# Optimization experiments

Measured on AMD Instinct MI355X. Metric: run time of the kernel, lower is better.

The kernel has to match this reference:

```python
import jax, jax.numpy as jnp
import numpy as np

COS_EPS = 1e-8    # torch.nn.CosineSimilarity default eps
NORM_EPS = 1e-12  # torch F.normalize default eps


def _cosine_gram(x, y):
    # Pairwise cosine similarity as a GEMM over row-normalized vectors,
    # matching torch: dot / max(|x|*|y|, eps). Avoids O(b^2*d) broadcast.
    dots = x @ y.T                               # [b, b]
    nx = jnp.linalg.norm(x, axis=1)              # [b]
    ny = jnp.linalg.norm(y, axis=1)              # [b]
    return dots / jnp.maximum(nx[:, None] * ny[None, :], COS_EPS)


def _row_normalize(g):
    # torch F.normalize(p=2, dim=1): x / max(||x||, eps)
    n = jnp.linalg.norm(g, axis=1, keepdims=True)
    return g / jnp.maximum(n, NORM_EPS)


def setup_inputs() -> dict:
    key = jax.random.key(0)
    k1, k2, k3, k4 = jax.random.split(key, 4)
    bsz, dim = 8192, 128
    return {
        "zxs": jax.random.normal(k1, (bsz, dim), dtype=jnp.float32),
        "zys": jax.random.normal(k2, (bsz, dim), dtype=jnp.float32),
        "zxt": jax.random.normal(k3, (bsz, dim), dtype=jnp.float32),
        "zyt": jax.random.normal(k4, (bsz, dim), dtype=jnp.float32),
        "temperature": jnp.asarray(0.5, dtype=jnp.float32),
    }


def reference(zxs, zys, zxt, zyt, temperature):
    bsz = zxs.shape[0]
    sim_s = _row_normalize(_cosine_gram(zxs, zys) / temperature)  # [b, b]
    sim_t = _row_normalize(_cosine_gram(zxt, zyt) / temperature)  # [b, b]
    g_diff = sim_t - sim_s
    loss = jnp.sum(g_diff * g_diff) / (bsz * bsz)
    return loss
```

## Files before the change

kernel.cpp:

```cpp
#include <hip/hip_runtime.h>
#include <hip/hip_bf16.h>


typedef __attribute__((ext_vector_type(8))) short short8;
typedef __attribute__((ext_vector_type(4))) float float4v;

#define BSZ 8192
#define DIM 128
#define NP  128
#define KROWS 64
#define PITCH 72
#define INV_B2 1.4901161193847656e-08f

__device__ __forceinline__ short f2bf(float x) {
    union { __hip_bfloat16 b; short s; } u;
    u.b = __float2bfloat16(x);
    return u.s;
}

__global__ __launch_bounds__(256, 3) void gram_g(
    const float* __restrict__ Yt, const float* __restrict__ Ys,
    float* __restrict__ partial)
{
    __shared__ short T[2][128 * PITCH];
    __shared__ float rsum[2][KROWS];
    __shared__ float invn[KROWS];

    const int tid   = threadIdx.x;
    const int lane  = tid & 63;
    const int wave  = tid >> 6;
    const int d     = tid & 127;
    const int khalf = tid >> 7;
    const int q     = lane >> 4;
    const int l15   = lane & 15;
    const int split = blockIdx.x;
    const int gram  = blockIdx.y;

    auto stage_mat = [&](int m, const float* __restrict__ Y) {
        float v[32];
        const float* base = Y + ((size_t)(split * KROWS + khalf * 32)) * DIM + d;
        #pragma unroll
        for (int i = 0; i < 32; ++i) v[i] = base[(size_t)i * DIM];

        #pragma unroll
        for (int i = 0; i < 32; ++i) {
            float ss = v[i] * v[i];
            #pragma unroll
            for (int off = 1; off < 64; off <<= 1) ss += __shfl_xor(ss, off);
            if (lane == 0) rsum[wave & 1][khalf * 32 + i] = ss;
        }
        __syncthreads();
        if (tid < KROWS) {
            float s = rsum[0][tid] + rsum[1][tid];
            invn[tid] = (s > 0.f) ? rsqrtf(s) : 0.f;
        }
        __syncthreads();

        #pragma unroll
        for (int g = 0; g < 4; ++g) {
            short8 pk;
            #pragma unroll
            for (int j = 0; j < 8; ++j) {
                int i = g * 8 + j;
                pk[j] = f2bf(v[i] * invn[khalf * 32 + i]);
            }
            *(short8*)&T[m][d * PITCH + khalf * 32 + g * 8] = pk;
        }
    };

    if (gram == 0) {
        stage_mat(0, Yt);
    } else if (gram == 1) {
        stage_mat(0, Ys);
    } else {
        stage_mat(0, Yt);
        __syncthreads();
        stage_mat(1, Ys);
    }
    __syncthreads();

    const short* TA = T[0];
    const short* TB = (gram == 2) ? T[1] : T[0];

    float4v acc[2][8];
    #pragma unroll
    for (int a = 0; a < 2; ++a)
        #pragma unroll
        for (int b = 0; b < 8; ++b) acc[a][b] = (float4v){0.f, 0.f, 0.f, 0.f};

    #pragma unroll
    for (int kk = 0; kk < 2; ++kk) {
        short8 fb[8], fa[2];
        #pragma unroll
        for (int s = 0; s < 8; ++s)
            fb[s] = *(const short8*)&TB[(s * 16 + l15) * PITCH + kk * 32 + q * 8];
        #pragma unroll
        for (int a = 0; a < 2; ++a)
            fa[a] = *(const short8*)&TA[((wave * 2 + a) * 16 + l15) * PITCH + kk * 32 + q * 8];
        #pragma unroll
        for (int a = 0; a < 2; ++a)
            #pragma unroll
            for (int b = 0; b < 8; ++b)
                acc[a][b] = __builtin_amdgcn_mfma_f32_16x16x32_bf16(
                    fa[a], fb[b], acc[a][b], 0, 0, 0);
    }

    float* P = partial + ((size_t)(gram * NP + split) << 14);
    #pragma unroll
    for (int a = 0; a < 2; ++a) {
        int strip = wave * 2 + a;
        #pragma unroll
        for (int b = 0; b < 8; ++b)
            #pragma unroll
            for (int r = 0; r < 4; ++r)
                P[((strip * 16 + q * 4 + r) << 7) + b * 16 + l15] = acc[a][b][r];
    }
}

__global__ __launch_bounds__(256) void reduce_g(
    const float* __restrict__ partial, __hip_bfloat16* __restrict__ Gb)
{
    int o = blockIdx.x * 256 + threadIdx.x;
    int g = o >> 14, rem = o & 16383;
    float s = 0.f;
    for (int b = 0; b < NP; ++b)
        s += partial[((size_t)(g * NP + b) << 14) + rem];
    int d1 = rem >> 7, d2 = rem & 127;
    Gb[(g << 14) + (d2 << 7) + d1] = __float2bfloat16(s);
}

__global__ __launch_bounds__(256) void quad_k(
    const float* __restrict__ Xt, const float* __restrict__ Xs,
    const __hip_bfloat16* __restrict__ Gb, float* __restrict__ out)
{
    const int tid  = threadIdx.x;
    const int lane = tid & 63;
    const int wave = tid >> 6;
    const int q    = lane >> 4;
    const int l15  = lane & 15;
    const int rbase = blockIdx.x * 64 + wave * 16;

    short8 At[4], As[4];
    #pragma unroll
    for (int kk = 0; kk < 4; ++kk) {
        const float* pt = Xt + (size_t)(rbase + l15) * DIM + kk * 32 + q * 8;
        const float* ps = Xs + (size_t)(rbase + l15) * DIM + kk * 32 + q * 8;
        float4 t0 = *(const float4*)pt, t1 = *(const float4*)(pt + 4);
        float4 s0 = *(const float4*)ps, s1 = *(const float4*)(ps + 4);
        short8 a, b;
        a[0]=f2bf(t0.x); a[1]=f2bf(t0.y); a[2]=f2bf(t0.z); a[3]=f2bf(t0.w);
        a[4]=f2bf(t1.x); a[5]=f2bf(t1.y); a[6]=f2bf(t1.z); a[7]=f2bf(t1.w);
        b[0]=f2bf(s0.x); b[1]=f2bf(s0.y); b[2]=f2bf(s0.z); b[3]=f2bf(s0.w);
        b[4]=f2bf(s1.x); b[5]=f2bf(s1.y); b[6]=f2bf(s1.z); b[7]=f2bf(s1.w);
        At[kk] = a; As[kk] = b;
    }

    float fA[4] = {0,0,0,0}, fB[4] = {0,0,0,0}, fC[4] = {0,0,0,0};
    const short* G = (const short*)Gb;

    #pragma unroll
    for (int nt = 0; nt < 8; ++nt) {
        int d2 = nt * 16 + l15;
        float4v qt = {0.f,0.f,0.f,0.f}, qs = qt, qc = qt;
        #pragma unroll
        for (int kk = 0; kk < 4; ++kk) {
            int off = (d2 << 7) + kk * 32 + q * 8;
            short8 Bt = *(const short8*)&G[off];
            short8 Bs = *(const short8*)&G[16384 + off];
            short8 Bm = *(const short8*)&G[32768 + off];
            qt = __builtin_amdgcn_mfma_f32_16x16x32_bf16(At[kk], Bt, qt, 0, 0, 0);
            qs = __builtin_amdgcn_mfma_f32_16x16x32_bf16(As[kk], Bs, qs, 0, 0, 0);
            qc = __builtin_amdgcn_mfma_f32_16x16x32_bf16(At[kk], Bm, qc, 0, 0, 0);
        }
        #pragma unroll
        for (int r = 0; r < 4; ++r) {
            int row = rbase + q * 4 + r;
            float xtv = Xt[(size_t)row * DIM + d2];
            float xsv = Xs[(size_t)row * DIM + d2];
            fA[r] += qt[r] * xtv;
            fB[r] += qs[r] * xsv;
            fC[r] += qc[r] * xsv;
        }
    }

    float wl = 0.f;
    #pragma unroll
    for (int r = 0; r < 4; ++r) {
        float A = fA[r], B = fB[r], C = fC[r];
        #pragma unroll
        for (int off = 1; off < 16; off <<= 1) {
            A += __shfl_xor(A, off);
            B += __shfl_xor(B, off);
            C += __shfl_xor(C, off);
        }
        float contrib = 2.f - 2.f * C * rsqrtf(A * B);
        wl += (l15 == 0) ? contrib : 0.f;
    }
    wl += __shfl_xor(wl, 16);
    wl += __shfl_xor(wl, 32);

    __shared__ float wred[4];
    if (lane == 0) wred[wave] = wl;
    __syncthreads();
    if (tid == 0)
        atomicAdd(out, (wred[0] + wred[1] + wred[2] + wred[3]) * INV_B2);
}

extern "C" void kernel_launch(void* const* d_in, const int* in_sizes, int n_in,
                              void* d_out, int out_size, void* d_ws, size_t ws_size,
                              hipStream_t stream) {
    const float* zxs = (const float*)d_in[0];
    const float* zys = (const float*)d_in[1];
    const float* zxt = (const float*)d_in[2];
    const float* zyt = (const float*)d_in[3];
    float* out = (float*)d_out;

    char* ws = (char*)d_ws;
    float* partial = (float*)ws;
    __hip_bfloat16* Gb = (__hip_bfloat16*)(ws + (size_t)3 * NP * 16384 * sizeof(float));

    hipMemsetAsync(out, 0, sizeof(float), stream);
    dim3 ggrid(NP, 3);
    gram_g  <<<ggrid, 256, 0, stream>>>(zyt, zys, partial);
    reduce_g<<<192,   256, 0, stream>>>(partial, Gb);
    quad_k  <<<128,   256, 0, stream>>>(zxt, zxs, Gb, out);
}
```

Before: 112.7 us.

## Split normalization into prep kernel, halve gram partials, drop memset

Adds a prep kernel that normalizes the Y rows once, converts them to bf16 and writes them transposed to workspace. The gram kernel then loads these fragments directly from global memory, using 512 threads and 128 K-rows per block. This removes the Yt/Ys normalization that the cross-gram blocks repeated and halves the partial buffer that reduce_g must sum. The output is now zeroed inside prep, replacing the memset. The cost is an extra launch plus a global round trip for the transposed data, and strided, uncached-looking global fragment loads in gram_g.

```diff
diff --git a/kernel.cpp b/kernel.cpp
--- a/kernel.cpp
+++ b/kernel.cpp
@@ -7,9 +7,7 @@
 
 #define BSZ 8192
 #define DIM 128
-#define NP  128
-#define KROWS 64
-#define PITCH 72
+#define NP  64
 #define INV_B2 1.4901161193847656e-08f
 
 __device__ __forceinline__ short f2bf(float x) {
@@ -18,103 +16,94 @@
     return u.s;
 }
 
-__global__ __launch_bounds__(256, 3) void gram_g(
+__global__ __launch_bounds__(256) void prep(
     const float* __restrict__ Yt, const float* __restrict__ Ys,
-    float* __restrict__ partial)
-{
-    __shared__ short T[2][128 * PITCH];
-    __shared__ float rsum[2][KROWS];
-    __shared__ float invn[KROWS];
+    short* __restrict__ YT, float* __restrict__ out)
+{
+    __shared__ float rsum[2][64];
+    __shared__ float invn[64];
 
     const int tid   = threadIdx.x;
     const int lane  = tid & 63;
     const int wave  = tid >> 6;
     const int d     = tid & 127;
     const int khalf = tid >> 7;
-    const int q     = lane >> 4;
-    const int l15   = lane & 15;
+    const int chunk = blockIdx.x;
+    const int mat   = blockIdx.y;
+    const float* Y  = mat ? Ys : Yt;
+
+    if (chunk == 0 && mat == 0 && tid == 0) out[0] = 0.f;
+
+    float v[32];
+    const float* base = Y + (size_t)(chunk * 64 + khalf * 32) * DIM + d;
+    #pragma unroll
+    for (int i = 0; i < 32; ++i) v[i] = base[(size_t)i * DIM];
+
+    #pragma unroll
+    for (int i = 0; i < 32; ++i) {
+        float ss = v[i] * v[i];
+        #pragma unroll
+        for (int off = 1; off < 64; off <<= 1) ss += __shfl_xor(ss, off);
+        if (lane == 0) rsum[wave & 1][khalf * 32 + i] = ss;
+    }
+    __syncthreads();
+    if (tid < 64) {
+        float s = rsum[0][tid] + rsum[1][tid];
+        invn[tid] = (s > 0.f) ? rsqrtf(s) : 0.f;
+    }
+    __syncthreads();
+
+    short* yt = YT + ((size_t)mat * 128 + d) * BSZ + chunk * 64 + khalf * 32;
+    #pragma unroll
+    for (int g = 0; g < 4; ++g) {
+        short8 pk;
+        #pragma unroll
+        for (int j = 0; j < 8; ++j) {
+            int i = g * 8 + j;
+            pk[j] = f2bf(v[i] * invn[khalf * 32 + i]);
+        }
+        *(short8*)&yt[g * 8] = pk;
+    }
+}
+
+__global__ __launch_bounds__(512) void gram_g(
+    const short* __restrict__ YT, float* __restrict__ partial)
+{
+    const int tid  = threadIdx.x;
+    const int lane = tid & 63;
+    const int s1   = tid >> 6;
+    const int q    = lane >> 4;
+    const int l15  = lane & 15;
     const int split = blockIdx.x;
     const int gram  = blockIdx.y;
 
-    auto stage_mat = [&](int m, const float* __restrict__ Y) {
-        float v[32];
-        const float* base = Y + ((size_t)(split * KROWS + khalf * 32)) * DIM + d;
-        #pragma unroll
-        for (int i = 0; i < 32; ++i) v[i] = base[(size_t)i * DIM];
-
-        #pragma unroll
-        for (int i = 0; i < 32; ++i) {
-            float ss = v[i] * v[i];
-            #pragma unroll
-            for (int off = 1; off < 64; off <<= 1) ss += __shfl_xor(ss, off);
-            if (lane == 0) rsum[wave & 1][khalf * 32 + i] = ss;
-        }
-        __syncthreads();
-        if (tid < KROWS) {
-            float s = rsum[0][tid] + rsum[1][tid];
-            invn[tid] = (s > 0.f) ? rsqrtf(s) : 0.f;
-        }
-        __syncthreads();
-
-        #pragma unroll
-        for (int g = 0; g < 4; ++g) {
-            short8 pk;
-            #pragma unroll
-            for (int j = 0; j < 8; ++j) {
-                int i = g * 8 + j;
-                pk[j] = f2bf(v[i] * invn[khalf * 32 + i]);
-            }
-            *(short8*)&T[m][d * PITCH + khalf * 32 + g * 8] = pk;
-        }
-    };
-
-    if (gram == 0) {
-        stage_mat(0, Yt);
-    } else if (gram == 1) {
-        stage_mat(0, Ys);
-    } else {
-        stage_mat(0, Yt);
-        __syncthreads();
-        stage_mat(1, Ys);
-    }
-    __syncthreads();
-
-    const short* TA = T[0];
-    const short* TB = (gram == 2) ? T[1] : T[0];
-
-    float4v acc[2][8];
-    #pragma unroll
-    for (int a = 0; a < 2; ++a)
-        #pragma unroll
-        for (int b = 0; b < 8; ++b) acc[a][b] = (float4v){0.f, 0.f, 0.f, 0.f};
-
-    #pragma unroll
-    for (int kk = 0; kk < 2; ++kk) {
-        short8 fb[8], fa[2];
-        #pragma unroll
-        for (int s = 0; s < 8; ++s)
-            fb[s] = *(const short8*)&TB[(s * 16 + l15) * PITCH + kk * 32 + q * 8];
-        #pragma unroll
-        for (int a = 0; a < 2; ++a)
-            fa[a] = *(const short8*)&TA[((wave * 2 + a) * 16 + l15) * PITCH + kk * 32 + q * 8];
-        #pragma unroll
-        for (int a = 0; a < 2; ++a)
-            #pragma unroll
-            for (int b = 0; b < 8; ++b)
-                acc[a][b] = __builtin_amdgcn_mfma_f32_16x16x32_bf16(
-                    fa[a], fb[b], acc[a][b], 0, 0, 0);
+    const short* Ta = (gram == 1) ? YT + (size_t)128 * BSZ : YT;
+    const short* Tb = (gram == 0) ? YT : YT + (size_t)128 * BSZ;
+    const int k0 = split * 128;
+
+    float4v acc[8];
+    #pragma unroll
+    for (int s2 = 0; s2 < 8; ++s2) acc[s2] = (float4v){0.f, 0.f, 0.f, 0.f};
+
+    #pragma unroll
+    for (int kk = 0; kk < 4; ++kk) {
+        const int ko = k0 + kk * 32 + q * 8;
+        short8 fa = *(const short8*)&Ta[(size_t)(s1 * 16 + l15) * BSZ + ko];
+        short8 fb[8];
+        #pragma unroll
+        for (int s2 = 0; s2 < 8; ++s2)
+            fb[s2] = *(const short8*)&Tb[(size_t)(s2 * 16 + l15) * BSZ + ko];
+        #pragma unroll
+        for (int s2 = 0; s2 < 8; ++s2)
+            acc[s2] = __builtin_amdgcn_mfma_f32_16x16x32_bf16(fa, fb[s2], acc[s2], 0, 0, 0);
     }
 
     float* P = partial + ((size_t)(gram * NP + split) << 14);
     #pragma unroll
-    for (int a = 0; a < 2; ++a) {
-        int strip = wave * 2 + a;
-        #pragma unroll
-        for (int b = 0; b < 8; ++b)
-            #pragma unroll
-            for (int r = 0; r < 4; ++r)
-                P[((strip * 16 + q * 4 + r) << 7) + b * 16 + l15] = acc[a][b][r];
-    }
+    for (int s2 = 0; s2 < 8; ++s2)
+        #pragma unroll
+        for (int r = 0; r < 4; ++r)
+            P[((s1 * 16 + q * 4 + r) << 7) + s2 * 16 + l15] = acc[s2][r];
 }
 
 __global__ __launch_bounds__(256) void reduce_g(
@@ -216,12 +205,13 @@
     float* out = (float*)d_out;
 
     char* ws = (char*)d_ws;
-    float* partial = (float*)ws;
-    __hip_bfloat16* Gb = (__hip_bfloat16*)(ws + (size_t)3 * NP * 16384 * sizeof(float));
-
-    hipMemsetAsync(out, 0, sizeof(float), stream);
-    dim3 ggrid(NP, 3);
-    gram_g  <<<ggrid, 256, 0, stream>>>(zyt, zys, partial);
-    reduce_g<<<192,   256, 0, stream>>>(partial, Gb);
-    quad_k  <<<128,   256, 0, stream>>>(zxt, zxs, Gb, out);
-}
+    short* YT = (short*)ws;
+    float* partial = (float*)(ws + (size_t)4 * 1024 * 1024);
+    __hip_bfloat16* Gb = (__hip_bfloat16*)(ws + (size_t)4 * 1024 * 1024
+                                              + (size_t)3 * NP * 16384 * sizeof(float));
+
+    prep    <<<dim3(128, 2), 256, 0, stream>>>(zyt, zys, YT, out);
+    gram_g  <<<dim3(NP, 3),  512, 0, stream>>>(YT, partial);
+    reduce_g<<<192,          256, 0, stream>>>(partial, Gb);
+    quad_k  <<<128,          256, 0, stream>>>(zxt, zxs, Gb, out);
+}
```

Measured after the change: 109.1 us. -3.2%, faster.
